# Kernel tuning notes

Hardware: AMD Instinct MI355X
Metric: run time of the kernel (lower is better)

The kernel has to match this reference:

```python
import jax, jax.numpy as jnp
import numpy as np

DQ = 256  # query feature size
DK = 256  # key feature size
DV = 256  # value feature size
B, SQ, SK = 4, 256, 256
D = DQ + DK  # MLP hidden width (512)


def setup_inputs() -> dict:
    key = jax.random.key(0)
    ks = jax.random.split(key, 7)
    Q = jax.random.normal(ks[0], (B, SQ, DQ), dtype=jnp.float32)
    K = jax.random.normal(ks[1], (B, SK, DK), dtype=jnp.float32)
    V = jax.random.normal(ks[2], (B, SK, DV), dtype=jnp.float32)
    # key-padding style mask: True = masked out. Keep at least the first key
    # unmasked so softmax rows are well-behaved.
    mask_out = jax.random.randint(ks[3], (B, 1, SK), 0, 2).astype(jnp.bool_)
    mask_out = mask_out.at[:, :, 0].set(False)
    # nn.Linear(D, D, bias=True): weight [D, D], bias [D]
    lim1 = 1.0 / np.sqrt(D)
    W1 = jax.random.uniform(ks[4], (D, D), minval=-lim1, maxval=lim1, dtype=jnp.float32)
    b1 = jax.random.uniform(ks[5], (D,), minval=-lim1, maxval=lim1, dtype=jnp.float32)
    # nn.Linear(D, 1, bias=False): weight [1, D] -> store as vector [D]
    W2 = jax.random.uniform(ks[6], (D,), minval=-lim1, maxval=lim1, dtype=jnp.float32)
    return {"Q": Q, "K": K, "V": V, "mask_out": mask_out, "W1": W1, "b1": b1, "W2": W2}


def reference(Q, K, V, mask_out, W1, b1, W2):
    # Concat-then-Linear splits: cat([q,k]) @ W1.T == q @ W1[:, :DQ].T + k @ W1[:, DQ:].T
    q_h = jnp.einsum('bqd,hd->bqh', Q, W1[:, :DQ])          # [B,SQ,D]
    k_h = jnp.einsum('bkd,hd->bkh', K, W1[:, DQ:])          # [B,SK,D]
    hidden = q_h[:, :, None, :] + k_h[:, None, :, :] + b1   # [B,SQ,SK,D]
    act = jax.nn.leaky_relu(hidden, negative_slope=0.01)
    scores = jnp.einsum('bqkh,h->bqk', act, W2)             # [B,SQ,SK]
    scores = jnp.where(mask_out, jnp.float32(-1e9), scores)
    attn = jax.nn.softmax(scores, axis=-1)
    return jnp.einsum('bqk,bkv->bqv', attn, V)              # [B,SQ,DV]
```

## Files before the change

### kernel.cpp

```cpp
#include <hip/hip_runtime.h>

#define HH_OFF 0
#define KT_OFF (1024 * 512)

typedef short short8 __attribute__((ext_vector_type(8)));
typedef float f32x4 __attribute__((ext_vector_type(4)));
typedef __fp16 half2v __attribute__((ext_vector_type(2)));

union S8 {
  short8 v;
  unsigned short s[8];
};
union H2U {
  half2v h;
  unsigned u;
};

__device__ __forceinline__ unsigned pkrtz(float a, float b) {
  H2U r;
  r.h = __builtin_amdgcn_cvt_pkrtz(a, b);
  return r.u;
}
__device__ __forceinline__ half2v uh(unsigned u) {
  H2U r;
  r.u = u;
  return r.h;
}
__device__ __forceinline__ float fdot2f(half2v a, half2v b, float c) {
#if __has_builtin(__builtin_amdgcn_fdot2)
  return __builtin_amdgcn_fdot2(a, b, c, false);
#else
  return c + (float)a.x * (float)b.x + (float)a.y * (float)b.y;
#endif
}
__device__ __forceinline__ half2v habs2(half2v a) {
  H2U r;
  r.h = a;
  r.u &= 0x7FFF7FFFu;
  return r.h;
}

__device__ __forceinline__ void cvt_split8(const float4& f0, const float4& f1,
                                           short8& hv8, short8& lv8) {
  float xs[8] = {f0.x, f0.y, f0.z, f0.w, f1.x, f1.y, f1.z, f1.w};
  S8 hv, lv;
#pragma unroll
  for (int e = 0; e < 8; ++e) {
    unsigned u = __float_as_uint(xs[e]);
    unsigned hu = u & 0xFFFF0000u;
    hv.s[e] = (unsigned short)(hu >> 16);
    float lo = xs[e] - __uint_as_float(hu);
    unsigned ul = __float_as_uint(lo);
    ul += 0x7FFFu + ((ul >> 16) & 1u);
    lv.s[e] = (unsigned short)(ul >> 16);
  }
  hv8 = hv.v;
  lv8 = lv.v;
}

__global__ __launch_bounds__(512) void gemm_k(const float* __restrict__ Q,
                                              const float* __restrict__ Kin,
                                              const float* __restrict__ W1,
                                              const float* __restrict__ b1,
                                              const void* __restrict__ maskp,
                                              float* __restrict__ hh,
                                              unsigned* __restrict__ kT2) {
  __shared__ short AH[64 * 32], AL[64 * 32], BH[64 * 32], BL[64 * 32];
  __shared__ int sflag, nkS, wsumS[4], kidxS[256];
  const int t = threadIdx.x;
  const int blk = blockIdx.x;
  const bool isK = blk >= 128;
  const float *A, *B;
  int lda, ldb, m0, n0, aoff, bb = 0, cchunk = 0;
  if (!isK) {
    int bm = blk >> 3, bn = blk & 7;
    m0 = bm * 64; n0 = bn * 64;
    A = Q;   lda = 256; aoff = 0;
    B = W1;  ldb = 512;
  } else {
    int t2 = blk - 128;
    int bm = t2 >> 4, bn = t2 & 15;
    m0 = bm * 64; n0 = bn * 64;
    A = W1;  lda = 512; aoff = 256;
    B = Kin; ldb = 256;
    bb = bn >> 2; cchunk = bn & 3;
    if (t == 0) sflag = 0;
    __syncthreads();
    if (t < 256) {
      const unsigned char* mb = (const unsigned char*)maskp;
      int nz = mb[t * 4 + 1] | mb[t * 4 + 2] | mb[t * 4 + 3];
      if (nz) atomicOr(&sflag, 1);
    }
    __syncthreads();
    const int w_ = t >> 6, lane_ = t & 63;
    bool act = false;
    int pre = 0;
    if (t < 256) {
      const int flag = sflag;
      const unsigned char* m8 = (const unsigned char*)maskp;
      const int* m32 = (const int*)maskp;
      act = flag ? (m8[bb * 256 + t] == 0) : (m32[bb * 256 + t] == 0);
      unsigned long long bal = __ballot(act);
      pre = __popcll(bal & ((1ull << lane_) - 1ull));
      if (lane_ == 0) wsumS[w_] = __popcll(bal);
    }
    __syncthreads();
    if (t < 256 && act) {
      int off = 0;
#pragma unroll
      for (int ww = 0; ww < 4; ++ww)
        if (ww < w_) off += wsumS[ww];
      kidxS[off + pre] = t;
    }
    if (t == 0) nkS = wsumS[0] + wsumS[1] + wsumS[2] + wsumS[3];
    __syncthreads();
    if (cchunk * 64 >= ((nkS + 63) & ~63)) return;
  }
  const int mat = t >> 8;
  const int cc = t & 255;
  const int sr = cc >> 2;
  const int c8 = (cc & 3) * 8;
  const float* srcbase;
  if (mat == 0) {
    srcbase = A + (size_t)(m0 + sr) * lda + aoff + c8;
  } else if (!isK) {
    srcbase = B + (size_t)(n0 + sr) * ldb + c8;
  } else {
    int jl = cchunk * 64 + sr;
    int kr = kidxS[jl < nkS ? jl : nkS - 1];
    srcbase = Kin + (size_t)(bb * 256 + kr) * 256 + c8;
  }
  short* dstH = (mat ? BH : AH) + sr * 32 + c8;
  short* dstL = (mat ? BL : AL) + sr * 32 + c8;

  const int w = t >> 6, lane = t & 63;
  const int wr = (w >> 2) * 32, wc = (w & 3) * 16;
  const int lane15 = lane & 15, lk8 = (lane >> 4) * 8;

  f32x4 acc[2] = {{0.f, 0.f, 0.f, 0.f}, {0.f, 0.f, 0.f, 0.f}};

  float4 f0 = *(const float4*)&srcbase[0];
  float4 f1 = *(const float4*)&srcbase[4];
  for (int ks = 0; ks < 8; ++ks) {
    short8 hv8, lv8;
    cvt_split8(f0, f1, hv8, lv8);
    __syncthreads();
    *(short8*)dstH = hv8;
    *(short8*)dstL = lv8;
    __syncthreads();
    if (ks < 7) {
      f0 = *(const float4*)&srcbase[(ks + 1) * 32];
      f1 = *(const float4*)&srcbase[(ks + 1) * 32 + 4];
    }
    short8 ah0 = *(const short8*)&AH[(wr + lane15) * 32 + lk8];
    short8 ah1 = *(const short8*)&AH[(wr + 16 + lane15) * 32 + lk8];
    short8 al0 = *(const short8*)&AL[(wr + lane15) * 32 + lk8];
    short8 al1 = *(const short8*)&AL[(wr + 16 + lane15) * 32 + lk8];
    short8 bh = *(const short8*)&BH[(wc + lane15) * 32 + lk8];
    short8 bl = *(const short8*)&BL[(wc + lane15) * 32 + lk8];
    acc[0] = __builtin_amdgcn_mfma_f32_16x16x32_bf16(ah0, bh, acc[0], 0, 0, 0);
    acc[1] = __builtin_amdgcn_mfma_f32_16x16x32_bf16(ah1, bh, acc[1], 0, 0, 0);
    acc[0] = __builtin_amdgcn_mfma_f32_16x16x32_bf16(ah0, bl, acc[0], 0, 0, 0);
    acc[1] = __builtin_amdgcn_mfma_f32_16x16x32_bf16(ah1, bl, acc[1], 0, 0, 0);
    acc[0] = __builtin_amdgcn_mfma_f32_16x16x32_bf16(al0, bh, acc[0], 0, 0, 0);
    acc[1] = __builtin_amdgcn_mfma_f32_16x16x32_bf16(al1, bh, acc[1], 0, 0, 0);
  }
  const int lg4 = (lane >> 4) * 4;
  if (!isK) {
#pragma unroll
    for (int i = 0; i < 2; ++i) {
#pragma unroll
      for (int reg = 0; reg < 4; ++reg) {
        int row = m0 + wr + i * 16 + lg4 + reg;
        hh[(size_t)row * 512 + n0 + wc + lane15] = acc[i][reg];
      }
    }
  } else {
    const int col = n0 + wc + lane15;
#pragma unroll
    for (int i = 0; i < 2; ++i) {
      int r0 = m0 + wr + i * 16 + lg4;
      float v0 = acc[i][0] + b1[r0 + 0];
      float v1 = acc[i][1] + b1[r0 + 1];
      float v2 = acc[i][2] + b1[r0 + 2];
      float v3 = acc[i][3] + b1[r0 + 3];
      int hp = r0 >> 1;
      kT2[(size_t)hp * 1024 + col] = pkrtz(v0, v1);
      kT2[(size_t)(hp + 1) * 1024 + col] = pkrtz(v2, v3);
    }
  }
}

__global__ __launch_bounds__(512) void attn_k(const float* __restrict__ hh,
                                              const unsigned* __restrict__ kT2,
                                              const float* __restrict__ V,
                                              const void* __restrict__ maskp,
                                              const float* __restrict__ W2,
                                              float* __restrict__ out) {
  __shared__ float smem[15296];
  __shared__ int sflag, nkS, wsumS[4];
  __shared__ int kidxS[256];
  float* att = smem;
  float* rowsum = smem + 1040;
  float* qlin = smem + 1044;
  float* qs = smem + 1048;
  float* w2s = smem + 3096;
  unsigned* w2p = (unsigned*)(smem + 3608);
  unsigned* qp = (unsigned*)(smem + 3864);
  float* sabs = smem + 4888;
  float* klin = smem + 13208;
  float* red = smem + 4888;

  const int t = threadIdx.x;
  const int blk = blockIdx.x;
  const int b = blk >> 6;
  const int q4 = blk & 63;
  const int w = t >> 6, lane = t & 63;

  if (t == 0) sflag = 0;
  {
    const float* qbase = hh + (size_t)(b * 256 + q4 * 4) * 512;
    int row = t >> 7, c4 = (t & 127) * 4;
    *(float4*)&qs[row * 512 + c4] = *(const float4*)&qbase[(size_t)row * 512 + c4];
    if (t < 128) *(float4*)&w2s[t * 4] = *(const float4*)&W2[t * 4];
  }
  __syncthreads();
  if (t < 256) {
    w2p[t] = pkrtz(w2s[2 * t], w2s[2 * t + 1]);
  }
  {
    int row = t >> 7, p0 = (t & 127) * 2;
    qp[row * 256 + p0] = pkrtz(qs[row * 512 + 2 * p0], qs[row * 512 + 2 * p0 + 1]);
    qp[row * 256 + p0 + 1] =
        pkrtz(qs[row * 512 + 2 * p0 + 2], qs[row * 512 + 2 * p0 + 3]);
  }
  if (t < 256) {
    const unsigned char* mb = (const unsigned char*)maskp;
    int nz = mb[t * 4 + 1] | mb[t * 4 + 2] | mb[t * 4 + 3];
    if (nz) atomicOr(&sflag, 1);
  }
  if (w < 4) {
    float p = 0.f;
#pragma unroll
    for (int u = 0; u < 8; ++u)
      p = fmaf(w2s[lane + 64 * u], qs[w * 512 + lane + 64 * u], p);
#pragma unroll
    for (int o = 32; o; o >>= 1) p += __shfl_xor(p, o, 64);
    if (lane == 0) qlin[w] = 0.505f * p;
  }
  __syncthreads();
  bool act = false;
  int pre = 0;
  if (t < 256) {
    const int flag = sflag;
    const unsigned char* m8 = (const unsigned char*)maskp;
    const int* m32 = (const int*)maskp;
    act = flag ? (m8[b * 256 + t] == 0) : (m32[b * 256 + t] == 0);
    unsigned long long bal = __ballot(act);
    pre = __popcll(bal & ((1ull << lane) - 1ull));
    if (lane == 0) wsumS[w] = __popcll(bal);
  }
  __syncthreads();
  if (t < 256 && act) {
    int off = 0;
#pragma unroll
    for (int ww = 0; ww < 4; ++ww)
      if (ww < w) off += wsumS[ww];
    kidxS[off + pre] = t;
  }
  if (t == 0) nkS = wsumS[0] + wsumS[1] + wsumS[2] + wsumS[3];
  __syncthreads();
  const int nk = nkS;
  const int nc64 = (nk + 63) >> 6;

  {
    const int gang = lane >> 4, li = lane & 15;
    const int hbase = w * 64 + gang * 16;
    const unsigned* kTb = kT2 + (size_t)b * 256;
#pragma unroll 1
    for (int cb = 0; cb < nc64; ++cb) {
      const int colo = cb * 64 + li * 4;
      float sa[4][4] = {};
      float kl4[4] = {};
#pragma unroll
      for (int hg = 0; hg < 4; ++hg) {
        const int h = hbase + hg * 4;
        const int hp = h >> 1;
        uint4 ua = *(const uint4*)&kTb[(size_t)hp * 1024 + colo];
        uint4 ub = *(const uint4*)&kTb[(size_t)(hp + 1) * 1024 + colo];
        uint2 wpp = *(const uint2*)&w2p[hp];
        half2v w01 = uh(wpp.x), w23 = uh(wpp.y);
        half2v q01[4], q23[4];
#pragma unroll
        for (int q = 0; q < 4; ++q) {
          uint2 qq = *(const uint2*)&qp[q * 256 + hp];
          q01[q] = uh(qq.x);
          q23[q] = uh(qq.y);
        }
        unsigned uac[4] = {ua.x, ua.y, ua.z, ua.w};
        unsigned ubc[4] = {ub.x, ub.y, ub.z, ub.w};
#pragma unroll
        for (int c = 0; c < 4; ++c) {
          half2v k01 = uh(uac[c]), k23 = uh(ubc[c]);
          kl4[c] = fdot2f(w01, k01, kl4[c]);
          kl4[c] = fdot2f(w23, k23, kl4[c]);
#pragma unroll
          for (int q = 0; q < 4; ++q) {
            sa[q][c] = fdot2f(w01, habs2(k01 + q01[q]), sa[q][c]);
            sa[q][c] = fdot2f(w23, habs2(k23 + q23[q]), sa[q][c]);
          }
        }
      }
#pragma unroll
      for (int q = 0; q < 4; ++q)
#pragma unroll
        for (int c = 0; c < 4; ++c) {
          sa[q][c] += __shfl_xor(sa[q][c], 16, 64);
          sa[q][c] += __shfl_xor(sa[q][c], 32, 64);
        }
#pragma unroll
      for (int c = 0; c < 4; ++c) {
        kl4[c] += __shfl_xor(kl4[c], 16, 64);
        kl4[c] += __shfl_xor(kl4[c], 32, 64);
      }
      if (gang == 0) {
#pragma unroll
        for (int q = 0; q < 4; ++q)
          *(float4*)&sabs[(w * 4 + q) * 260 + colo] =
              make_float4(sa[q][0], sa[q][1], sa[q][2], sa[q][3]);
        *(float4*)&klin[w * 260 + colo] =
            make_float4(kl4[0], kl4[1], kl4[2], kl4[3]);
      }
    }
  }
  __syncthreads();
  if (t < 256) {
#pragma unroll
    for (int q = 0; q < 4; ++q) att[q * 260 + t] = -1e9f;
  }
  __syncthreads();
  if (t < nk) {
    const int realk = kidxS[t];
    float kls = 0.f;
#pragma unroll
    for (int ww = 0; ww < 8; ++ww) kls += klin[ww * 260 + t];
    kls *= 0.505f;
#pragma unroll
    for (int q = 0; q < 4; ++q) {
      float v = 0.f;
#pragma unroll
      for (int ww = 0; ww < 8; ++ww) v += sabs[(ww * 4 + q) * 260 + t];
      att[q * 260 + realk] = qlin[q] + kls + 0.495f * v;
    }
  }
  __syncthreads();
  if (w < 4) {
    float m = -1e30f;
#pragma unroll
    for (int u = 0; u < 4; ++u) m = fmaxf(m, att[w * 260 + lane + 64 * u]);
#pragma unroll
    for (int o = 32; o; o >>= 1) m = fmaxf(m, __shfl_xor(m, o, 64));
    float ssum = 0.f;
#pragma unroll
    for (int u = 0; u < 4; ++u) {
      float e = __expf(att[w * 260 + lane + 64 * u] - m);
      att[w * 260 + lane + 64 * u] = e;
      ssum += e;
    }
#pragma unroll
    for (int o = 32; o; o >>= 1) ssum += __shfl_xor(ssum, o, 64);
    if (lane == 0) rowsum[w] = ssum;
  }
  __syncthreads();
  {
    const int v0 = lane * 4;
    const float* Vb = V + (size_t)b * 65536;
    float acc[4][4] = {};
    for (int i = w; i < nk; i += 8) {
      int k = kidxS[i];
      float4 vv = *(const float4*)&Vb[(size_t)k * 256 + v0];
      float aw[4];
#pragma unroll
      for (int q = 0; q < 4; ++q) aw[q] = att[q * 260 + k];
#pragma unroll
      for (int q = 0; q < 4; ++q) {
        acc[q][0] = fmaf(aw[q], vv.x, acc[q][0]);
        acc[q][1] = fmaf(aw[q], vv.y, acc[q][1]);
        acc[q][2] = fmaf(aw[q], vv.z, acc[q][2]);
        acc[q][3] = fmaf(aw[q], vv.w, acc[q][3]);
      }
    }
#pragma unroll
    for (int q = 0; q < 4; ++q)
      *(float4*)&red[(w * 4 + q) * 264 + v0] =
          make_float4(acc[q][0], acc[q][1], acc[q][2], acc[q][3]);
  }
  __syncthreads();
#pragma unroll
  for (int s = 0; s < 2; ++s) {
    int id = t + s * 512;
    int row = id >> 8, col = id & 255;
    float v = 0.f;
#pragma unroll
    for (int g = 0; g < 8; ++g) v += red[(g * 4 + row) * 264 + col];
    out[((size_t)b * 256 + q4 * 4 + row) * 256 + col] = v / rowsum[row];
  }
}

extern "C" void kernel_launch(void* const* d_in, const int* in_sizes, int n_in,
                              void* d_out, int out_size, void* d_ws,
                              size_t ws_size, hipStream_t stream) {
  const float* Q = (const float*)d_in[0];
  const float* K = (const float*)d_in[1];
  const float* V = (const float*)d_in[2];
  const void* mask = d_in[3];
  const float* W1 = (const float*)d_in[4];
  const float* b1 = (const float*)d_in[5];
  const float* W2 = (const float*)d_in[6];
  float* ws = (float*)d_ws;
  float* hh = ws + HH_OFF;
  unsigned* kT2 = (unsigned*)(ws + KT_OFF);
  float* out = (float*)d_out;

  gemm_k<<<dim3(256), dim3(512), 0, stream>>>(Q, K, W1, b1, mask, hh, kT2);
  attn_k<<<dim3(256), dim3(512), 0, stream>>>(hh, kT2, V, mask, W2, out);
}
```

Baseline: 29.19 us.

## Fuse GEMM and attention kernels with global atomic flag dependencies

Merges the projection GEMM kernel and the attention kernel into one 512-block launch. The first 256 blocks compute the hidden projections and bump per-tile completion counters. The attention blocks do their mask and setup work first, then spin on those counters before reading the results. This removes the kernel-boundary gap and lets setup overlap with the GEMM, but adds a memset launch, spin-waits, and a risk of deadlock if consumer blocks get scheduled before producers.

```diff
diff --git a/kernel.cpp b/kernel.cpp
--- a/kernel.cpp
+++ b/kernel.cpp
@@ -2,6 +2,7 @@
 
 #define HH_OFF 0
 #define KT_OFF (1024 * 512)
+#define FLAG_OFF (KT_OFF + 256 * 1024)
 
 typedef short short8 __attribute__((ext_vector_type(8)));
 typedef float f32x4 __attribute__((ext_vector_type(4)));
@@ -58,148 +59,168 @@
   lv8 = lv.v;
 }
 
-__global__ __launch_bounds__(512) void gemm_k(const float* __restrict__ Q,
-                                              const float* __restrict__ Kin,
-                                              const float* __restrict__ W1,
-                                              const float* __restrict__ b1,
-                                              const void* __restrict__ maskp,
-                                              float* __restrict__ hh,
-                                              unsigned* __restrict__ kT2) {
-  __shared__ short AH[64 * 32], AL[64 * 32], BH[64 * 32], BL[64 * 32];
-  __shared__ int sflag, nkS, wsumS[4], kidxS[256];
+__global__ __launch_bounds__(512, 4) void fused_k(
+    const float* __restrict__ Q, const float* __restrict__ Kin,
+    const float* __restrict__ V, const void* __restrict__ maskp,
+    const float* __restrict__ W1, const float* __restrict__ b1,
+    const float* __restrict__ W2, float* __restrict__ hh,
+    unsigned* __restrict__ kT2, int* __restrict__ flags,
+    float* __restrict__ out) {
+  __shared__ __align__(16) float smem[15296];
+  __shared__ int sflag, nkS, wsumS[4];
+  __shared__ int kidxS[256];
   const int t = threadIdx.x;
   const int blk = blockIdx.x;
-  const bool isK = blk >= 128;
-  const float *A, *B;
-  int lda, ldb, m0, n0, aoff, bb = 0, cchunk = 0;
-  if (!isK) {
-    int bm = blk >> 3, bn = blk & 7;
-    m0 = bm * 64; n0 = bn * 64;
-    A = Q;   lda = 256; aoff = 0;
-    B = W1;  ldb = 512;
-  } else {
-    int t2 = blk - 128;
-    int bm = t2 >> 4, bn = t2 & 15;
-    m0 = bm * 64; n0 = bn * 64;
-    A = W1;  lda = 512; aoff = 256;
-    B = Kin; ldb = 256;
-    bb = bn >> 2; cchunk = bn & 3;
-    if (t == 0) sflag = 0;
-    __syncthreads();
-    if (t < 256) {
-      const unsigned char* mb = (const unsigned char*)maskp;
-      int nz = mb[t * 4 + 1] | mb[t * 4 + 2] | mb[t * 4 + 3];
-      if (nz) atomicOr(&sflag, 1);
-    }
-    __syncthreads();
-    const int w_ = t >> 6, lane_ = t & 63;
-    bool act = false;
-    int pre = 0;
-    if (t < 256) {
-      const int flag = sflag;
-      const unsigned char* m8 = (const unsigned char*)maskp;
-      const int* m32 = (const int*)maskp;
-      act = flag ? (m8[bb * 256 + t] == 0) : (m32[bb * 256 + t] == 0);
-      unsigned long long bal = __ballot(act);
-      pre = __popcll(bal & ((1ull << lane_) - 1ull));
-      if (lane_ == 0) wsumS[w_] = __popcll(bal);
-    }
-    __syncthreads();
-    if (t < 256 && act) {
-      int off = 0;
-#pragma unroll
-      for (int ww = 0; ww < 4; ++ww)
-        if (ww < w_) off += wsumS[ww];
-      kidxS[off + pre] = t;
-    }
-    if (t == 0) nkS = wsumS[0] + wsumS[1] + wsumS[2] + wsumS[3];
-    __syncthreads();
-    if (cchunk * 64 >= ((nkS + 63) & ~63)) return;
-  }
-  const int mat = t >> 8;
-  const int cc = t & 255;
-  const int sr = cc >> 2;
-  const int c8 = (cc & 3) * 8;
-  const float* srcbase;
-  if (mat == 0) {
-    srcbase = A + (size_t)(m0 + sr) * lda + aoff + c8;
-  } else if (!isK) {
-    srcbase = B + (size_t)(n0 + sr) * ldb + c8;
-  } else {
-    int jl = cchunk * 64 + sr;
-    int kr = kidxS[jl < nkS ? jl : nkS - 1];
-    srcbase = Kin + (size_t)(bb * 256 + kr) * 256 + c8;
-  }
-  short* dstH = (mat ? BH : AH) + sr * 32 + c8;
-  short* dstL = (mat ? BL : AL) + sr * 32 + c8;
-
   const int w = t >> 6, lane = t & 63;
-  const int wr = (w >> 2) * 32, wc = (w & 3) * 16;
-  const int lane15 = lane & 15, lk8 = (lane >> 4) * 8;
-
-  f32x4 acc[2] = {{0.f, 0.f, 0.f, 0.f}, {0.f, 0.f, 0.f, 0.f}};
-
-  float4 f0 = *(const float4*)&srcbase[0];
-  float4 f1 = *(const float4*)&srcbase[4];
-  for (int ks = 0; ks < 8; ++ks) {
-    short8 hv8, lv8;
-    cvt_split8(f0, f1, hv8, lv8);
-    __syncthreads();
-    *(short8*)dstH = hv8;
-    *(short8*)dstL = lv8;
-    __syncthreads();
-    if (ks < 7) {
-      f0 = *(const float4*)&srcbase[(ks + 1) * 32];
-      f1 = *(const float4*)&srcbase[(ks + 1) * 32 + 4];
-    }
-    short8 ah0 = *(const short8*)&AH[(wr + lane15) * 32 + lk8];
-    short8 ah1 = *(const short8*)&AH[(wr + 16 + lane15) * 32 + lk8];
-    short8 al0 = *(const short8*)&AL[(wr + lane15) * 32 + lk8];
-    short8 al1 = *(const short8*)&AL[(wr + 16 + lane15) * 32 + lk8];
-    short8 bh = *(const short8*)&BH[(wc + lane15) * 32 + lk8];
-    short8 bl = *(const short8*)&BL[(wc + lane15) * 32 + lk8];
-    acc[0] = __builtin_amdgcn_mfma_f32_16x16x32_bf16(ah0, bh, acc[0], 0, 0, 0);
-    acc[1] = __builtin_amdgcn_mfma_f32_16x16x32_bf16(ah1, bh, acc[1], 0, 0, 0);
-    acc[0] = __builtin_amdgcn_mfma_f32_16x16x32_bf16(ah0, bl, acc[0], 0, 0, 0);
-    acc[1] = __builtin_amdgcn_mfma_f32_16x16x32_bf16(ah1, bl, acc[1], 0, 0, 0);
-    acc[0] = __builtin_amdgcn_mfma_f32_16x16x32_bf16(al0, bh, acc[0], 0, 0, 0);
-    acc[1] = __builtin_amdgcn_mfma_f32_16x16x32_bf16(al1, bh, acc[1], 0, 0, 0);
-  }
-  const int lg4 = (lane >> 4) * 4;
-  if (!isK) {
-#pragma unroll
-    for (int i = 0; i < 2; ++i) {
-#pragma unroll
-      for (int reg = 0; reg < 4; ++reg) {
-        int row = m0 + wr + i * 16 + lg4 + reg;
-        hh[(size_t)row * 512 + n0 + wc + lane15] = acc[i][reg];
-      }
-    }
-  } else {
-    const int col = n0 + wc + lane15;
-#pragma unroll
-    for (int i = 0; i < 2; ++i) {
-      int r0 = m0 + wr + i * 16 + lg4;
-      float v0 = acc[i][0] + b1[r0 + 0];
-      float v1 = acc[i][1] + b1[r0 + 1];
-      float v2 = acc[i][2] + b1[r0 + 2];
-      float v3 = acc[i][3] + b1[r0 + 3];
-      int hp = r0 >> 1;
-      kT2[(size_t)hp * 1024 + col] = pkrtz(v0, v1);
-      kT2[(size_t)(hp + 1) * 1024 + col] = pkrtz(v2, v3);
-    }
-  }
-}
-
-__global__ __launch_bounds__(512) void attn_k(const float* __restrict__ hh,
-                                              const unsigned* __restrict__ kT2,
-                                              const float* __restrict__ V,
-                                              const void* __restrict__ maskp,
-                                              const float* __restrict__ W2,
-                                              float* __restrict__ out) {
-  __shared__ float smem[15296];
-  __shared__ int sflag, nkS, wsumS[4];
-  __shared__ int kidxS[256];
+  int* hhdone = flags;
+  int* ktdone = flags + 16;
+
+  if (blk < 256) {
+    const bool isK = blk >= 128;
+    const float *A, *B;
+    int lda, ldb, m0, n0, aoff, bb = 0, cchunk = 0;
+    if (!isK) {
+      int bm = blk >> 3, bn = blk & 7;
+      m0 = bm * 64; n0 = bn * 64;
+      A = Q;   lda = 256; aoff = 0;
+      B = W1;  ldb = 512;
+    } else {
+      int t2 = blk - 128;
+      int bm = t2 >> 4, bn = t2 & 15;
+      m0 = bm * 64; n0 = bn * 64;
+      A = W1;  lda = 512; aoff = 256;
+      B = Kin; ldb = 256;
+      bb = bn >> 2; cchunk = bn & 3;
+      if (t == 0) sflag = 0;
+      __syncthreads();
+      if (t < 256) {
+        const unsigned char* mb = (const unsigned char*)maskp;
+        int nz = mb[t * 4 + 1] | mb[t * 4 + 2] | mb[t * 4 + 3];
+        if (nz) atomicOr(&sflag, 1);
+      }
+      __syncthreads();
+      bool act = false;
+      int pre = 0;
+      if (t < 256) {
+        const int flag = sflag;
+        const unsigned char* m8 = (const unsigned char*)maskp;
+        const int* m32 = (const int*)maskp;
+        act = flag ? (m8[bb * 256 + t] == 0) : (m32[bb * 256 + t] == 0);
+        unsigned long long bal = __ballot(act);
+        pre = __popcll(bal & ((1ull << lane) - 1ull));
+        if (lane == 0) wsumS[w] = __popcll(bal);
+      }
+      __syncthreads();
+      if (t < 256 && act) {
+        int off = 0;
+#pragma unroll
+        for (int ww = 0; ww < 4; ++ww)
+          if (ww < w) off += wsumS[ww];
+        kidxS[off + pre] = t;
+      }
+      if (t == 0) nkS = wsumS[0] + wsumS[1] + wsumS[2] + wsumS[3];
+      __syncthreads();
+      if (cchunk * 64 >= ((nkS + 63) & ~63)) {
+        if (t == 0)
+          __hip_atomic_fetch_add(&ktdone[bb], 1, __ATOMIC_RELAXED,
+                                 __HIP_MEMORY_SCOPE_AGENT);
+        return;
+      }
+    }
+    short* AH = (short*)smem;
+    short* AL = (short*)(smem + 1024);
+    short* BH = (short*)(smem + 2048);
+    short* BL = (short*)(smem + 3072);
+    const int mat = t >> 8;
+    const int cc = t & 255;
+    const int sr = cc >> 2;
+    const int c8 = (cc & 3) * 8;
+    const float* srcbase;
+    if (mat == 0) {
+      srcbase = A + (size_t)(m0 + sr) * lda + aoff + c8;
+    } else if (!isK) {
+      srcbase = B + (size_t)(n0 + sr) * ldb + c8;
+    } else {
+      int jl = cchunk * 64 + sr;
+      int kr = kidxS[jl < nkS ? jl : nkS - 1];
+      srcbase = Kin + (size_t)(bb * 256 + kr) * 256 + c8;
+    }
+    short* dstH = (mat ? BH : AH) + sr * 32 + c8;
+    short* dstL = (mat ? BL : AL) + sr * 32 + c8;
+
+    const int wr = (w >> 2) * 32, wc = (w & 3) * 16;
+    const int lane15 = lane & 15, lk8 = (lane >> 4) * 8;
+
+    f32x4 acc[2] = {{0.f, 0.f, 0.f, 0.f}, {0.f, 0.f, 0.f, 0.f}};
+
+    float4 f0 = *(const float4*)&srcbase[0];
+    float4 f1 = *(const float4*)&srcbase[4];
+    for (int ks = 0; ks < 8; ++ks) {
+      short8 hv8, lv8;
+      cvt_split8(f0, f1, hv8, lv8);
+      __syncthreads();
+      *(short8*)dstH = hv8;
+      *(short8*)dstL = lv8;
+      __syncthreads();
+      if (ks < 7) {
+        f0 = *(const float4*)&srcbase[(ks + 1) * 32];
+        f1 = *(const float4*)&srcbase[(ks + 1) * 32 + 4];
+      }
+      short8 ah0 = *(const short8*)&AH[(wr + lane15) * 32 + lk8];
+      short8 ah1 = *(const short8*)&AH[(wr + 16 + lane15) * 32 + lk8];
+      short8 al0 = *(const short8*)&AL[(wr + lane15) * 32 + lk8];
+      short8 al1 = *(const short8*)&AL[(wr + 16 + lane15) * 32 + lk8];
+      short8 bh = *(const short8*)&BH[(wc + lane15) * 32 + lk8];
+      short8 bl = *(const short8*)&BL[(wc + lane15) * 32 + lk8];
+      acc[0] = __builtin_amdgcn_mfma_f32_16x16x32_bf16(ah0, bh, acc[0], 0, 0, 0);
+      acc[1] = __builtin_amdgcn_mfma_f32_16x16x32_bf16(ah1, bh, acc[1], 0, 0, 0);
+      acc[0] = __builtin_amdgcn_mfma_f32_16x16x32_bf16(ah0, bl, acc[0], 0, 0, 0);
+      acc[1] = __builtin_amdgcn_mfma_f32_16x16x32_bf16(ah1, bl, acc[1], 0, 0, 0);
+      acc[0] = __builtin_amdgcn_mfma_f32_16x16x32_bf16(al0, bh, acc[0], 0, 0, 0);
+      acc[1] = __builtin_amdgcn_mfma_f32_16x16x32_bf16(al1, bh, acc[1], 0, 0, 0);
+    }
+    const int lg4 = (lane >> 4) * 4;
+    if (!isK) {
+#pragma unroll
+      for (int i = 0; i < 2; ++i) {
+#pragma unroll
+        for (int reg = 0; reg < 4; ++reg) {
+          int row = m0 + wr + i * 16 + lg4 + reg;
+          hh[(size_t)row * 512 + n0 + wc + lane15] = acc[i][reg];
+        }
+      }
+      __syncthreads();
+      if (t == 0) {
+        __threadfence();
+        __hip_atomic_fetch_add(&hhdone[blk >> 3], 1, __ATOMIC_RELAXED,
+                               __HIP_MEMORY_SCOPE_AGENT);
+      }
+    } else {
+      const int col = n0 + wc + lane15;
+#pragma unroll
+      for (int i = 0; i < 2; ++i) {
+        int r0 = m0 + wr + i * 16 + lg4;
+        float v0 = acc[i][0] + b1[r0 + 0];
+        float v1 = acc[i][1] + b1[r0 + 1];
+        float v2 = acc[i][2] + b1[r0 + 2];
+        float v3 = acc[i][3] + b1[r0 + 3];
+        int hp = r0 >> 1;
+        kT2[(size_t)hp * 1024 + col] = pkrtz(v0, v1);
+        kT2[(size_t)(hp + 1) * 1024 + col] = pkrtz(v2, v3);
+      }
+      __syncthreads();
+      if (t == 0) {
+        __threadfence();
+        __hip_atomic_fetch_add(&ktdone[bb], 1, __ATOMIC_RELAXED,
+                               __HIP_MEMORY_SCOPE_AGENT);
+      }
+    }
+    return;
+  }
+
+  const int ab = blk - 256;
+  const int b = ab >> 6;
+  const int q4 = ab & 63;
   float* att = smem;
   float* rowsum = smem + 1040;
   float* qlin = smem + 1044;
@@ -211,43 +232,15 @@
   float* klin = smem + 13208;
   float* red = smem + 4888;
 
-  const int t = threadIdx.x;
-  const int blk = blockIdx.x;
-  const int b = blk >> 6;
-  const int q4 = blk & 63;
-  const int w = t >> 6, lane = t & 63;
-
   if (t == 0) sflag = 0;
-  {
-    const float* qbase = hh + (size_t)(b * 256 + q4 * 4) * 512;
-    int row = t >> 7, c4 = (t & 127) * 4;
-    *(float4*)&qs[row * 512 + c4] = *(const float4*)&qbase[(size_t)row * 512 + c4];
-    if (t < 128) *(float4*)&w2s[t * 4] = *(const float4*)&W2[t * 4];
-  }
-  __syncthreads();
-  if (t < 256) {
-    w2p[t] = pkrtz(w2s[2 * t], w2s[2 * t + 1]);
-  }
-  {
-    int row = t >> 7, p0 = (t & 127) * 2;
-    qp[row * 256 + p0] = pkrtz(qs[row * 512 + 2 * p0], qs[row * 512 + 2 * p0 + 1]);
-    qp[row * 256 + p0 + 1] =
-        pkrtz(qs[row * 512 + 2 * p0 + 2], qs[row * 512 + 2 * p0 + 3]);
-  }
+  if (t < 128) *(float4*)&w2s[t * 4] = *(const float4*)&W2[t * 4];
+  __syncthreads();
   if (t < 256) {
     const unsigned char* mb = (const unsigned char*)maskp;
     int nz = mb[t * 4 + 1] | mb[t * 4 + 2] | mb[t * 4 + 3];
     if (nz) atomicOr(&sflag, 1);
   }
-  if (w < 4) {
-    float p = 0.f;
-#pragma unroll
-    for (int u = 0; u < 8; ++u)
-      p = fmaf(w2s[lane + 64 * u], qs[w * 512 + lane + 64 * u], p);
-#pragma unroll
-    for (int o = 32; o; o >>= 1) p += __shfl_xor(p, o, 64);
-    if (lane == 0) qlin[w] = 0.505f * p;
-  }
+  if (t < 256) w2p[t] = pkrtz(w2s[2 * t], w2s[2 * t + 1]);
   __syncthreads();
   bool act = false;
   int pre = 0;
@@ -269,9 +262,47 @@
     kidxS[off + pre] = t;
   }
   if (t == 0) nkS = wsumS[0] + wsumS[1] + wsumS[2] + wsumS[3];
+
+  if (t == 0) {
+    const int bmq = b * 4 + (q4 >> 4);
+    while (__hip_atomic_load(&hhdone[bmq], __ATOMIC_RELAXED,
+                             __HIP_MEMORY_SCOPE_AGENT) < 8) {
+      __builtin_amdgcn_s_sleep(2);
+    }
+    __threadfence();
+  }
   __syncthreads();
   const int nk = nkS;
   const int nc64 = (nk + 63) >> 6;
+  {
+    const float* qbase = hh + (size_t)(b * 256 + q4 * 4) * 512;
+    int row = t >> 7, c4 = (t & 127) * 4;
+    *(float4*)&qs[row * 512 + c4] = *(const float4*)&qbase[(size_t)row * 512 + c4];
+  }
+  __syncthreads();
+  {
+    int row = t >> 7, p0 = (t & 127) * 2;
+    qp[row * 256 + p0] = pkrtz(qs[row * 512 + 2 * p0], qs[row * 512 + 2 * p0 + 1]);
+    qp[row * 256 + p0 + 1] =
+        pkrtz(qs[row * 512 + 2 * p0 + 2], qs[row * 512 + 2 * p0 + 3]);
+  }
+  if (w < 4) {
+    float p = 0.f;
+#pragma unroll
+    for (int u = 0; u < 8; ++u)
+      p = fmaf(w2s[lane + 64 * u], qs[w * 512 + lane + 64 * u], p);
+#pragma unroll
+    for (int o = 32; o; o >>= 1) p += __shfl_xor(p, o, 64);
+    if (lane == 0) qlin[w] = 0.505f * p;
+  }
+  if (t == 0) {
+    while (__hip_atomic_load(&ktdone[b], __ATOMIC_RELAXED,
+                             __HIP_MEMORY_SCOPE_AGENT) < 32) {
+      __builtin_amdgcn_s_sleep(2);
+    }
+    __threadfence();
+  }
+  __syncthreads();
 
   {
     const int gang = lane >> 4, li = lane & 15;
@@ -420,8 +451,10 @@
   float* ws = (float*)d_ws;
   float* hh = ws + HH_OFF;
   unsigned* kT2 = (unsigned*)(ws + KT_OFF);
+  int* flags = (int*)(ws + FLAG_OFF);
   float* out = (float*)d_out;
 
-  gemm_k<<<dim3(256), dim3(512), 0, stream>>>(Q, K, W1, b1, mask, hh, kT2);
-  attn_k<<<dim3(256), dim3(512), 0, stream>>>(hh, kT2, V, mask, W2, out);
-}
+  hipMemsetAsync(flags, 0, 128, stream);
+  fused_k<<<dim3(512), dim3(512), 0, stream>>>(Q, K, V, mask, W1, b1, W2, hh,
+                                               kT2, flags, out);
+}
```

Measured after the change: 65.08 us. +122.9%, slower.
